# Performance work log

Measured on AMD Instinct MI355X. Metric: run time of the kernel, lower is better.

Reference implementation:

```python
import jax, jax.numpy as jnp
import numpy as np

N_NODES = 100000
N_EDGES = 1600000
D_IN, D_H, D_OUT = 256, 128, 128


def setup_inputs() -> dict:
    key = jax.random.key(0)
    ks = jax.random.split(key, 8)
    x = jax.random.normal(ks[0], (N_NODES, D_IN), dtype=jnp.float32)
    edge_index = jax.random.randint(ks[1], (2, N_EDGES), 0, N_NODES, dtype=jnp.int64)
    def glorot(k, fan_in, fan_out):
        s = jnp.sqrt(6.0 / (fan_in + fan_out))
        return jax.random.uniform(k, (fan_in, fan_out), jnp.float32, -s, s)
    W1 = glorot(ks[2], D_IN, D_H)
    b1 = jnp.zeros((D_H,), jnp.float32)
    W2 = glorot(ks[3], D_H, D_H)
    b2 = jnp.zeros((D_H,), jnp.float32)
    W3 = glorot(ks[4], D_H, D_OUT)
    b3 = jnp.zeros((D_OUT,), jnp.float32)
    return {"x": x, "edge_index": edge_index,
            "W1": W1, "b1": b1, "W2": W2, "b2": b2, "W3": W3, "b3": b3}


def _gcn_norm(edge_index, n_nodes):
    # PyG GCNConv: add self-loops, symmetric normalization D^-1/2 (A+I) D^-1/2
    loop = jnp.arange(n_nodes, dtype=edge_index.dtype)
    src = jnp.concatenate([edge_index[0], loop])  # source j
    dst = jnp.concatenate([edge_index[1], loop])  # target i
    deg = jax.ops.segment_sum(jnp.ones_like(dst, dtype=jnp.float32), dst,
                              num_segments=n_nodes)
    dinv = jnp.where(deg > 0, jax.lax.rsqrt(deg), 0.0)
    norm = dinv[src] * dinv[dst]  # [E+N]
    return src, dst, norm


def _gcn_conv(h, W, b, src, dst, norm, n_nodes):
    h = h @ W                                   # [N, d_out] transform first
    msg = h[src] * norm[:, None]                # gather + edge-weight
    out = jax.ops.segment_sum(msg, dst, num_segments=n_nodes)  # scatter-add
    return out + b


def reference(x, edge_index, W1, b1, W2, b2, W3, b3):
    n = x.shape[0]
    src, dst, norm = _gcn_norm(edge_index, n)
    h = jax.nn.relu(_gcn_conv(x, W1, b1, src, dst, norm, n))
    h = jax.nn.relu(_gcn_conv(h, W2, b2, src, dst, norm, n))
    return _gcn_conv(h, W3, b3, src, dst, norm, n)
```

## Files before the change

kernel.cpp:

```cpp
#include <hip/hip_runtime.h>
#include <hip/hip_fp16.h>
#include <math.h>


#define N_NODES 100000
#define N_EDGES 1600000

typedef _Float16 f16x8 __attribute__((ext_vector_type(8)));
typedef float    f32x4 __attribute__((ext_vector_type(4)));


__global__ __launch_bounds__(256) void k_zero_int(int* __restrict__ p, int n) {
    int i = blockIdx.x * 256 + threadIdx.x;
    if (i < n) p[i] = 0;
}

__global__ __launch_bounds__(256) void k_count(const int* __restrict__ dst, int* __restrict__ cnt, int E) {
    int e = blockIdx.x * 256 + threadIdx.x;
    if (e < E) atomicAdd(&cnt[dst[e]], 1);
}

__global__ __launch_bounds__(256) void k_scan_block(const int* __restrict__ cnt, int* __restrict__ excl,
                                                    int* __restrict__ bsum, int n) {
    __shared__ int s[256];
    int i = blockIdx.x * 256 + threadIdx.x;
    int v = (i < n) ? ((cnt[i] + 7) & ~7) : 0;
    s[threadIdx.x] = v;
    __syncthreads();
    #pragma unroll
    for (int off = 1; off < 256; off <<= 1) {
        int t = (threadIdx.x >= (unsigned)off) ? s[threadIdx.x - off] : 0;
        __syncthreads();
        s[threadIdx.x] += t;
        __syncthreads();
    }
    if (i < n) excl[i] = s[threadIdx.x] - v;
    if (threadIdx.x == 255) bsum[blockIdx.x] = s[255];
}

__global__ __launch_bounds__(512) void k_scan_partials(int* __restrict__ bsum, int nb) {
    __shared__ int s[512];
    int tid = threadIdx.x;
    int v = (tid < nb) ? bsum[tid] : 0;
    s[tid] = v;
    __syncthreads();
    #pragma unroll
    for (int off = 1; off < 512; off <<= 1) {
        int t = (tid >= (unsigned)off) ? s[tid - off] : 0;
        __syncthreads();
        s[tid] += t;
        __syncthreads();
    }
    if (tid < nb) bsum[tid] = s[tid] - v;
}

__global__ __launch_bounds__(256) void k_finalize(const int* __restrict__ excl, const int* __restrict__ bsum,
                                                  const int* __restrict__ cnt, int* __restrict__ rowptr,
                                                  int* __restrict__ fill, float* __restrict__ dinv, int n) {
    int i = blockIdx.x * 256 + threadIdx.x;
    if (i < n) {
        int rp = excl[i] + bsum[i >> 8];
        rowptr[i] = rp;
        fill[i]   = rp;
        dinv[i]   = rsqrtf((float)(cnt[i] + 1));
    }
}

__global__ __launch_bounds__(256) void k_init_csr(int* __restrict__ csr, int n, unsigned int* __restrict__ phz) {
    int i = blockIdx.x * 256 + threadIdx.x;
    if (i < n) csr[i] = N_NODES;
    if (blockIdx.x == 0 && threadIdx.x < 64) phz[threadIdx.x] = 0;
}

__global__ __launch_bounds__(256) void k_fill_edges(const int* __restrict__ src, const int* __restrict__ dst,
                                                    int* __restrict__ fill, int* __restrict__ csr,
                                                    int E, int lo, int hi) {
    int e = blockIdx.x * 256 + threadIdx.x;
    if (e < E) {
        int d = dst[e];
        if (d >= lo && d < hi) {
            int p = atomicAdd(&fill[d], 1);
            csr[p] = src[e];
        }
    }
}

__global__ __launch_bounds__(256) void k_wpack(const float* __restrict__ W, _Float16* __restrict__ Wpk, int K) {
    int j = blockIdx.x * 256 + threadIdx.x;
    if (j < K * 128) {
        int i  = j & 7;
        int l  = (j >> 3) & 63;
        int tc = (j >> 9) & 7;
        int c  = j >> 12;
        int col = tc * 16 + (l & 15);
        int k   = c * 32 + (l >> 4) * 8 + i;
        float w = W[(size_t)k * 128 + col];
        _Float16 h = (_Float16)w;
        Wpk[j] = h;
        Wpk[(size_t)K * 128 + j] = (_Float16)(w - (float)h);
    }
}


template <int K>
__global__ __launch_bounds__(256) void k_gemm_mfma(const float* __restrict__ X,
                                                   const _Float16* __restrict__ Wpk,
                                                   const float* __restrict__ dinv,
                                                   _Float16* __restrict__ Y, int n) {
    constexpr int NC = K / 32;
    __shared__ float sX[64 * 32];
    const int t    = threadIdx.x;
    const int wave = t >> 6;
    const int lane = t & 63;
    const int lrow = lane & 15;
    const int kgrp = lane >> 4;
    const int row0 = blockIdx.x * 64;
    const int R    = wave * 16 + lrow;
    const _Float16* __restrict__ Wlo = Wpk + (size_t)K * 128;

    const int rs0 = t >> 3,        gs = t & 7;
    const int rs1 = (t >> 3) + 32;
    const int gc0 = (gs ^ (rs0 & 7)) << 2;
    const int gc1 = (gs ^ (rs1 & 7)) << 2;
    const int gr0 = row0 + rs0, gr1 = row0 + rs1;
    const bool ok0 = gr0 < n, ok1 = gr1 < n;
    const float* __restrict__ xr0 = X + (size_t)gr0 * K;
    const float* __restrict__ xr1 = X + (size_t)gr1 * K;

    f32x4 acc[8];
    #pragma unroll
    for (int i = 0; i < 8; ++i) acc[i] = (f32x4){0.f, 0.f, 0.f, 0.f};

    const float4 z4 = make_float4(0.f, 0.f, 0.f, 0.f);
    float4 rv0 = ok0 ? *(const float4*)&xr0[gc0] : z4;
    float4 rv1 = ok1 ? *(const float4*)&xr1[gc1] : z4;
    *(float4*)&sX[(rs0 * 8 + gs) * 4] = rv0;
    *(float4*)&sX[(rs1 * 8 + gs) * 4] = rv1;
    __syncthreads();

    #pragma unroll
    for (int c = 0; c < NC; ++c) {
        if (c + 1 < NC) {
            rv0 = ok0 ? *(const float4*)&xr0[(c + 1) * 32 + gc0] : z4;
            rv1 = ok1 ? *(const float4*)&xr1[(c + 1) * 32 + gc1] : z4;
        }
        float4 x0 = *(const float4*)&sX[(R * 8 + ((kgrp * 2)     ^ (R & 7))) * 4];
        float4 x1 = *(const float4*)&sX[(R * 8 + ((kgrp * 2 + 1) ^ (R & 7))) * 4];
        float xs[8] = {x0.x, x0.y, x0.z, x0.w, x1.x, x1.y, x1.z, x1.w};
        f16x8 ah, al;
        #pragma unroll
        for (int i = 0; i < 8; ++i) {
            _Float16 h = (_Float16)xs[i];
            ah[i] = h;
            al[i] = (_Float16)(xs[i] - (float)h);
        }
        const size_t wb = ((size_t)(c * 8) * 64 + lane) * 8;
        #pragma unroll
        for (int tc = 0; tc < 8; ++tc) {
            f16x8 bh = *(const f16x8*)(Wpk + wb + (size_t)tc * 512);
            f16x8 bl = *(const f16x8*)(Wlo + wb + (size_t)tc * 512);
            acc[tc] = __builtin_amdgcn_mfma_f32_16x16x32_f16(ah, bh, acc[tc], 0, 0, 0);
            acc[tc] = __builtin_amdgcn_mfma_f32_16x16x32_f16(al, bh, acc[tc], 0, 0, 0);
            acc[tc] = __builtin_amdgcn_mfma_f32_16x16x32_f16(ah, bl, acc[tc], 0, 0, 0);
        }
        if (c + 1 < NC) {
            __syncthreads();
            *(float4*)&sX[(rs0 * 8 + gs) * 4] = rv0;
            *(float4*)&sX[(rs1 * 8 + gs) * 4] = rv1;
            __syncthreads();
        }
    }

    #pragma unroll
    for (int r = 0; r < 4; ++r) {
        int grow = row0 + wave * 16 + kgrp * 4 + r;
        if (grow < n) {
            float dv = dinv[grow];
            _Float16* yr = Y + (size_t)grow * 128 + lrow;
            #pragma unroll
            for (int tc = 0; tc < 8; ++tc) yr[tc * 16] = (_Float16)(dv * acc[tc][r]);
        }
    }
}


__device__ __forceinline__ void acc8(float a[8], uint4 u) {
    float2 p;
    p = __half22float2(*(__half2*)&u.x); a[0] += p.x; a[1] += p.y;
    p = __half22float2(*(__half2*)&u.y); a[2] += p.x; a[3] += p.y;
    p = __half22float2(*(__half2*)&u.z); a[4] += p.x; a[5] += p.y;
    p = __half22float2(*(__half2*)&u.w); a[6] += p.x; a[7] += p.y;
}

template <bool RELU>
__global__ __launch_bounds__(256) void k_agg(const __half* __restrict__ H, const int* __restrict__ rowptr,
                                             const int* __restrict__ cnt, const int* __restrict__ csr,
                                             const float* __restrict__ dinv, const float* __restrict__ bias,
                                             float* __restrict__ out, int n) {
    const int lane  = threadIdx.x & 63;
    const int q     = lane >> 4;
    const int fl    = lane & 15;
    const int wave0 = (int)((blockIdx.x * 256 + threadIdx.x) >> 6);
    const int nwave = (int)((gridDim.x * 256) >> 6);
    const uint4* __restrict__ Hu = (const uint4*)H;
    const float4 b0 = *(const float4*)&bias[fl * 8];
    const float4 b1 = *(const float4*)&bias[fl * 8 + 4];

    const int nquad = n >> 2;
    for (int g = wave0; g < nquad; g += nwave) {
        const int node = g * 4 + q;
        float a[8];
        {
            uint4 u = Hu[(size_t)node * 16 + fl];
            float2 p;
            p = __half22float2(*(__half2*)&u.x); a[0] = p.x; a[1] = p.y;
            p = __half22float2(*(__half2*)&u.y); a[2] = p.x; a[3] = p.y;
            p = __half22float2(*(__half2*)&u.z); a[4] = p.x; a[5] = p.y;
            p = __half22float2(*(__half2*)&u.w); a[6] = p.x; a[7] = p.y;
        }

        const int c0 = rowptr[node];
        const int cn = cnt[node];
        for (int e8 = 0; e8 < cn; e8 += 8) {
            const int4* qp = (const int4*)(csr + c0 + e8);
            int4 qa = qp[0], qb = qp[1];
            uint4 u0 = Hu[(size_t)qa.x * 16 + fl];
            uint4 u1 = Hu[(size_t)qa.y * 16 + fl];
            uint4 u2 = Hu[(size_t)qa.z * 16 + fl];
            uint4 u3 = Hu[(size_t)qa.w * 16 + fl];
            uint4 u4 = Hu[(size_t)qb.x * 16 + fl];
            uint4 u5 = Hu[(size_t)qb.y * 16 + fl];
            uint4 u6 = Hu[(size_t)qb.z * 16 + fl];
            uint4 u7 = Hu[(size_t)qb.w * 16 + fl];
            acc8(a, u0); acc8(a, u1); acc8(a, u2); acc8(a, u3);
            acc8(a, u4); acc8(a, u5); acc8(a, u6); acc8(a, u7);
        }

        const float dv = dinv[node];
        float4 o0, o1;
        o0.x = fmaf(dv, a[0], b0.x); o0.y = fmaf(dv, a[1], b0.y);
        o0.z = fmaf(dv, a[2], b0.z); o0.w = fmaf(dv, a[3], b0.w);
        o1.x = fmaf(dv, a[4], b1.x); o1.y = fmaf(dv, a[5], b1.y);
        o1.z = fmaf(dv, a[6], b1.z); o1.w = fmaf(dv, a[7], b1.w);
        if (RELU) {
            o0.x = fmaxf(o0.x, 0.f); o0.y = fmaxf(o0.y, 0.f);
            o0.z = fmaxf(o0.z, 0.f); o0.w = fmaxf(o0.w, 0.f);
            o1.x = fmaxf(o1.x, 0.f); o1.y = fmaxf(o1.y, 0.f);
            o1.z = fmaxf(o1.z, 0.f); o1.w = fmaxf(o1.w, 0.f);
        }
        *(float4*)&out[(size_t)node * 128 + fl * 8]     = o0;
        *(float4*)&out[(size_t)node * 128 + fl * 8 + 4] = o1;
    }
}


extern "C" void kernel_launch(void* const* d_in, const int* in_sizes, int n_in,
                              void* d_out, int out_size, void* d_ws, size_t ws_size,
                              hipStream_t stream) {
    const float* x  = (const float*)d_in[0];
    const int*   ei = (const int*)d_in[1];
    const float* W1 = (const float*)d_in[2];
    const float* b1 = (const float*)d_in[3];
    const float* W2 = (const float*)d_in[4];
    const float* b2 = (const float*)d_in[5];
    const float* W3 = (const float*)d_in[6];
    const float* b3 = (const float*)d_in[7];
    float* out = (float*)d_out;

    const int N = N_NODES, E = N_EDGES;
    const int EP = E + 7 * N + 64;
    const int* src = ei;
    const int* dst = ei + E;

    char* w = (char*)d_ws;
    auto alloc = [&](size_t bytes) -> void* {
        void* p = (void*)w;
        w += (bytes + 255) & ~(size_t)255;
        return p;
    };
    int*      cnt    = (int*)alloc((size_t)N * 4);
    int*      excl   = (int*)alloc((size_t)N * 4);
    int*      bsum   = (int*)alloc(4096);
    int*      rowptr = (int*)alloc((size_t)N * 4);
    int*      fill   = (int*)alloc((size_t)N * 4);
    float*    dinv   = (float*)alloc((size_t)N * 4);
    int*      csr    = (int*)alloc((size_t)EP * 4);
    _Float16* Ph     = (_Float16*)alloc((size_t)(N + 8) * 128 * 2);
    _Float16* Wpk    = (_Float16*)alloc((size_t)2 * 256 * 128 * 2);
    float*    Q      = out;

    const int nbN = (N + 255) / 256;
    const int nbE = (E + 255) / 256;
    const int nbP = (EP + 255) / 256;

    k_zero_int<<<nbN, 256, 0, stream>>>(cnt, N);
    k_count<<<nbE, 256, 0, stream>>>(dst, cnt, E);
    k_scan_block<<<nbN, 256, 0, stream>>>(cnt, excl, bsum, N);
    k_scan_partials<<<1, 512, 0, stream>>>(bsum, nbN);
    k_finalize<<<nbN, 256, 0, stream>>>(excl, bsum, cnt, rowptr, fill, dinv, N);
    k_init_csr<<<nbP, 256, 0, stream>>>(csr, EP, (unsigned int*)(Ph + (size_t)N * 128));
    for (int r = 0; r < 4; ++r) {
        int lo = r * (N / 4);
        int hi = (r == 3) ? N : (r + 1) * (N / 4);
        k_fill_edges<<<nbE, 256, 0, stream>>>(src, dst, fill, csr, E, lo, hi);
    }

    const int gemm_grid = (N + 63) / 64;
    const int agg_grid  = 2048;

    k_wpack<<<(256 * 128 + 255) / 256, 256, 0, stream>>>(W1, Wpk, 256);
    k_gemm_mfma<256><<<gemm_grid, 256, 0, stream>>>(x, Wpk, dinv, Ph, N);
    k_agg<true><<<agg_grid, 256, 0, stream>>>((const __half*)Ph, rowptr, cnt, csr, dinv, b1, Q, N);
    k_wpack<<<(128 * 128 + 255) / 256, 256, 0, stream>>>(W2, Wpk, 128);
    k_gemm_mfma<128><<<gemm_grid, 256, 0, stream>>>(Q, Wpk, dinv, Ph, N);
    k_agg<true><<<agg_grid, 256, 0, stream>>>((const __half*)Ph, rowptr, cnt, csr, dinv, b2, Q, N);
    k_wpack<<<(128 * 128 + 255) / 256, 256, 0, stream>>>(W3, Wpk, 128);
    k_gemm_mfma<128><<<gemm_grid, 256, 0, stream>>>(Q, Wpk, dinv, Ph, N);
    k_agg<false><<<agg_grid, 256, 0, stream>>>((const __half*)Ph, rowptr, cnt, csr, dinv, b3, out, N);
}
```

Measured before the change: 464.3 us.

## Store hidden activations in fp16 and split degree counting into node-range passes

Intermediate layer outputs from aggregation are now written as fp16 into a workspace buffer, and a new fp16-input MFMA GEMM reads them directly. The A operand is no longer split into hi/lo parts; only the weight hi/lo split remains. This halves the activation traffic between aggregation and the next GEMM. Degree counting is also split into four launches that each cover a quarter of the destination range, so the atomics hit a more localized slice of memory. The cost is fp16 rounding of the hidden activations and extra passes over the edge list for counting.

```diff
diff --git a/kernel.cpp b/kernel.cpp
--- a/kernel.cpp
+++ b/kernel.cpp
@@ -15,9 +15,13 @@
     if (i < n) p[i] = 0;
 }
 
-__global__ __launch_bounds__(256) void k_count(const int* __restrict__ dst, int* __restrict__ cnt, int E) {
+__global__ __launch_bounds__(256) void k_count(const int* __restrict__ dst, int* __restrict__ cnt,
+                                               int E, int lo, int hi) {
     int e = blockIdx.x * 256 + threadIdx.x;
-    if (e < E) atomicAdd(&cnt[dst[e]], 1);
+    if (e < E) {
+        int d = dst[e];
+        if (d >= lo && d < hi) atomicAdd(&cnt[d], 1);
+    }
 }
 
 __global__ __launch_bounds__(256) void k_scan_block(const int* __restrict__ cnt, int* __restrict__ excl,
@@ -103,10 +107,10 @@
 
 
 template <int K>
-__global__ __launch_bounds__(256) void k_gemm_mfma(const float* __restrict__ X,
-                                                   const _Float16* __restrict__ Wpk,
-                                                   const float* __restrict__ dinv,
-                                                   _Float16* __restrict__ Y, int n) {
+__global__ __launch_bounds__(256) void k_gemm_f32(const float* __restrict__ X,
+                                                  const _Float16* __restrict__ Wpk,
+                                                  const float* __restrict__ dinv,
+                                                  _Float16* __restrict__ Y, int n) {
     constexpr int NC = K / 32;
     __shared__ float sX[64 * 32];
     const int t    = threadIdx.x;
@@ -184,6 +188,67 @@
 }
 
 
+template <int K>
+__global__ __launch_bounds__(256) void k_gemm_f16(const _Float16* __restrict__ X,
+                                                  const _Float16* __restrict__ Wpk,
+                                                  const float* __restrict__ dinv,
+                                                  _Float16* __restrict__ Y, int n) {
+    constexpr int NC = K / 32;
+    __shared__ unsigned int sX[64 * 20];
+    const int t    = threadIdx.x;
+    const int wave = t >> 6;
+    const int lane = t & 63;
+    const int lrow = lane & 15;
+    const int kgrp = lane >> 4;
+    const int row0 = blockIdx.x * 64;
+    const int R    = wave * 16 + lrow;
+    const _Float16* __restrict__ Wlo = Wpk + (size_t)K * 128;
+
+    const int sr = t >> 2, sg = t & 3;
+    const bool sok = row0 + sr < n;
+    const unsigned int* __restrict__ xrow = (const unsigned int*)(X + (size_t)(row0 + sr) * K);
+
+    f32x4 acc[8];
+    #pragma unroll
+    for (int i = 0; i < 8; ++i) acc[i] = (f32x4){0.f, 0.f, 0.f, 0.f};
+
+    const uint4 zu = make_uint4(0, 0, 0, 0);
+    uint4 rv = sok ? *(const uint4*)&xrow[sg * 4] : zu;
+    *(uint4*)&sX[sr * 20 + sg * 4] = rv;
+    __syncthreads();
+
+    #pragma unroll
+    for (int c = 0; c < NC; ++c) {
+        if (c + 1 < NC) rv = sok ? *(const uint4*)&xrow[(c + 1) * 16 + sg * 4] : zu;
+        f16x8 a = *(const f16x8*)&sX[R * 20 + kgrp * 4];
+        const size_t wb = ((size_t)(c * 8) * 64 + lane) * 8;
+        #pragma unroll
+        for (int tc = 0; tc < 8; ++tc) {
+            f16x8 bh = *(const f16x8*)(Wpk + wb + (size_t)tc * 512);
+            f16x8 bl = *(const f16x8*)(Wlo + wb + (size_t)tc * 512);
+            acc[tc] = __builtin_amdgcn_mfma_f32_16x16x32_f16(a, bh, acc[tc], 0, 0, 0);
+            acc[tc] = __builtin_amdgcn_mfma_f32_16x16x32_f16(a, bl, acc[tc], 0, 0, 0);
+        }
+        if (c + 1 < NC) {
+            __syncthreads();
+            *(uint4*)&sX[sr * 20 + sg * 4] = rv;
+            __syncthreads();
+        }
+    }
+
+    #pragma unroll
+    for (int r = 0; r < 4; ++r) {
+        int grow = row0 + wave * 16 + kgrp * 4 + r;
+        if (grow < n) {
+            float dv = dinv[grow];
+            _Float16* yr = Y + (size_t)grow * 128 + lrow;
+            #pragma unroll
+            for (int tc = 0; tc < 8; ++tc) yr[tc * 16] = (_Float16)(dv * acc[tc][r]);
+        }
+    }
+}
+
+
 __device__ __forceinline__ void acc8(float a[8], uint4 u) {
     float2 p;
     p = __half22float2(*(__half2*)&u.x); a[0] += p.x; a[1] += p.y;
@@ -192,11 +257,11 @@
     p = __half22float2(*(__half2*)&u.w); a[6] += p.x; a[7] += p.y;
 }
 
-template <bool RELU>
+template <bool RELU, bool OUTF16>
 __global__ __launch_bounds__(256) void k_agg(const __half* __restrict__ H, const int* __restrict__ rowptr,
                                              const int* __restrict__ cnt, const int* __restrict__ csr,
                                              const float* __restrict__ dinv, const float* __restrict__ bias,
-                                             float* __restrict__ out, int n) {
+                                             void* __restrict__ out, int n) {
     const int lane  = threadIdx.x & 63;
     const int q     = lane >> 4;
     const int fl    = lane & 15;
@@ -237,19 +302,25 @@
         }
 
         const float dv = dinv[node];
-        float4 o0, o1;
-        o0.x = fmaf(dv, a[0], b0.x); o0.y = fmaf(dv, a[1], b0.y);
-        o0.z = fmaf(dv, a[2], b0.z); o0.w = fmaf(dv, a[3], b0.w);
-        o1.x = fmaf(dv, a[4], b1.x); o1.y = fmaf(dv, a[5], b1.y);
-        o1.z = fmaf(dv, a[6], b1.z); o1.w = fmaf(dv, a[7], b1.w);
+        float o[8];
+        o[0] = fmaf(dv, a[0], b0.x); o[1] = fmaf(dv, a[1], b0.y);
+        o[2] = fmaf(dv, a[2], b0.z); o[3] = fmaf(dv, a[3], b0.w);
+        o[4] = fmaf(dv, a[4], b1.x); o[5] = fmaf(dv, a[5], b1.y);
+        o[6] = fmaf(dv, a[6], b1.z); o[7] = fmaf(dv, a[7], b1.w);
         if (RELU) {
-            o0.x = fmaxf(o0.x, 0.f); o0.y = fmaxf(o0.y, 0.f);
-            o0.z = fmaxf(o0.z, 0.f); o0.w = fmaxf(o0.w, 0.f);
-            o1.x = fmaxf(o1.x, 0.f); o1.y = fmaxf(o1.y, 0.f);
-            o1.z = fmaxf(o1.z, 0.f); o1.w = fmaxf(o1.w, 0.f);
-        }
-        *(float4*)&out[(size_t)node * 128 + fl * 8]     = o0;
-        *(float4*)&out[(size_t)node * 128 + fl * 8 + 4] = o1;
+            #pragma unroll
+            for (int i = 0; i < 8; ++i) o[i] = fmaxf(o[i], 0.f);
+        }
+        if (OUTF16) {
+            f16x8 hv;
+            #pragma unroll
+            for (int i = 0; i < 8; ++i) hv[i] = (_Float16)o[i];
+            *(f16x8*)((_Float16*)out + (size_t)node * 128 + fl * 8) = hv;
+        } else {
+            float* op = (float*)out + (size_t)node * 128 + fl * 8;
+            *(float4*)&op[0] = make_float4(o[0], o[1], o[2], o[3]);
+            *(float4*)&op[4] = make_float4(o[4], o[5], o[6], o[7]);
+        }
     }
 }
 
@@ -286,15 +357,19 @@
     float*    dinv   = (float*)alloc((size_t)N * 4);
     int*      csr    = (int*)alloc((size_t)EP * 4);
     _Float16* Ph     = (_Float16*)alloc((size_t)(N + 8) * 128 * 2);
+    _Float16* Qh     = (_Float16*)alloc((size_t)N * 128 * 2);
     _Float16* Wpk    = (_Float16*)alloc((size_t)2 * 256 * 128 * 2);
-    float*    Q      = out;
 
     const int nbN = (N + 255) / 256;
     const int nbE = (E + 255) / 256;
     const int nbP = (EP + 255) / 256;
 
     k_zero_int<<<nbN, 256, 0, stream>>>(cnt, N);
-    k_count<<<nbE, 256, 0, stream>>>(dst, cnt, E);
+    for (int r = 0; r < 4; ++r) {
+        int lo = r * (N / 4);
+        int hi = (r == 3) ? N : (r + 1) * (N / 4);
+        k_count<<<nbE, 256, 0, stream>>>(dst, cnt, E, lo, hi);
+    }
     k_scan_block<<<nbN, 256, 0, stream>>>(cnt, excl, bsum, N);
     k_scan_partials<<<1, 512, 0, stream>>>(bsum, nbN);
     k_finalize<<<nbN, 256, 0, stream>>>(excl, bsum, cnt, rowptr, fill, dinv, N);
@@ -309,12 +384,12 @@
     const int agg_grid  = 2048;
 
     k_wpack<<<(256 * 128 + 255) / 256, 256, 0, stream>>>(W1, Wpk, 256);
-    k_gemm_mfma<256><<<gemm_grid, 256, 0, stream>>>(x, Wpk, dinv, Ph, N);
-    k_agg<true><<<agg_grid, 256, 0, stream>>>((const __half*)Ph, rowptr, cnt, csr, dinv, b1, Q, N);
+    k_gemm_f32<256><<<gemm_grid, 256, 0, stream>>>(x, Wpk, dinv, Ph, N);
+    k_agg<true, true><<<agg_grid, 256, 0, stream>>>((const __half*)Ph, rowptr, cnt, csr, dinv, b1, Qh, N);
     k_wpack<<<(128 * 128 + 255) / 256, 256, 0, stream>>>(W2, Wpk, 128);
-    k_gemm_mfma<128><<<gemm_grid, 256, 0, stream>>>(Q, Wpk, dinv, Ph, N);
-    k_agg<true><<<agg_grid, 256, 0, stream>>>((const __half*)Ph, rowptr, cnt, csr, dinv, b2, Q, N);
+    k_gemm_f16<128><<<gemm_grid, 256, 0, stream>>>(Qh, Wpk, dinv, Ph, N);
+    k_agg<true, true><<<agg_grid, 256, 0, stream>>>((const __half*)Ph, rowptr, cnt, csr, dinv, b2, Qh, N);
     k_wpack<<<(128 * 128 + 255) / 256, 256, 0, stream>>>(W3, Wpk, 128);
-    k_gemm_mfma<128><<<gemm_grid, 256, 0, stream>>>(Q, Wpk, dinv, Ph, N);
-    k_agg<false><<<agg_grid, 256, 0, stream>>>((const __half*)Ph, rowptr, cnt, csr, dinv, b3, out, N);
-}
+    k_gemm_f16<128><<<gemm_grid, 256, 0, stream>>>(Qh, Wpk, dinv, Ph, N);
+    k_agg<false, false><<<agg_grid, 256, 0, stream>>>((const __half*)Ph, rowptr, cnt, csr, dinv, b3, out, N);
+}
```

New measurement: 476.2 us. +2.6%, slower.
